# Kernel tuning notes

Measured on AMD Instinct MI355X. Metric: run time of the kernel, lower is better.

Reference implementation:

```python
import jax, jax.numpy as jnp
import numpy as np

N, D, H, F = 50000, 128, 8, 512
HD = D // H
EPS_BN = 1e-5


def _batchnorm(x, gamma, beta):
    # BatchNorm1d in training mode: per-feature batch stats over node dim
    m = x.mean(axis=0)
    v = x.var(axis=0)
    return (x - m) * jax.lax.rsqrt(v + EPS_BN) * gamma + beta


def setup_inputs() -> dict:
    key = jax.random.key(0)
    ks = jax.random.split(key, 12)
    s = 0.05
    return {
        "src": jax.random.normal(ks[0], (N, D), jnp.float32),
        "edge_index": jax.random.randint(ks[1], (2, 800000), 0, N, jnp.int64),
        "q_w": jax.random.normal(ks[2], (D, D), jnp.float32) * s,
        "q_b": jnp.zeros((D,), jnp.float32),
        "k_w": jax.random.normal(ks[3], (D, D), jnp.float32) * s,
        "v_w": jax.random.normal(ks[4], (D, D), jnp.float32) * s,
        "out_w": jax.random.normal(ks[5], (D, D), jnp.float32) * s,
        "out_b": jnp.zeros((D,), jnp.float32),
        "g1": jnp.ones((D,), jnp.float32),
        "b1": jnp.zeros((D,), jnp.float32),
        "lin1_w": jax.random.normal(ks[6], (F, D), jnp.float32) * s,
        "lin1_b": jnp.zeros((F,), jnp.float32),
        "lin2_w": jax.random.normal(ks[7], (D, F), jnp.float32) * s,
        "lin2_b": jnp.zeros((D,), jnp.float32),
        "g2": jnp.ones((D,), jnp.float32),
        "b2": jnp.zeros((D,), jnp.float32),
    }


def reference(src, edge_index, q_w, q_b, k_w, v_w, out_w, out_b,
              g1, b1, lin1_w, lin1_b, lin2_w, lin2_b, g2, b2):
    n = src.shape[0]
    # add self loops, then attention edge index is (dst=edge[1], src=edge[0])
    loops = jnp.arange(n, dtype=edge_index.dtype)
    ei = jnp.concatenate([edge_index, jnp.stack([loops, loops])], axis=1)
    e_src, e_dst = ei[0], ei[1]  # message flows e_src -> e_dst; query index = e_dst

    scaling = float(HD) ** (-0.5)
    q = ((src @ q_w.T + q_b) * scaling).reshape(n, H, HD)
    k = (src @ k_w.T).reshape(n, H, HD)
    v = (src @ v_w.T).reshape(n, H, HD)

    # per-edge scores [E, H]
    w = jnp.einsum("ehd,ehd->eh", q[e_dst], k[e_src])
    # deterministic segment softmax over edges grouped by destination node
    mx = jax.ops.segment_max(w, e_dst, num_segments=n)
    ex = jnp.exp(w - mx[e_dst])
    den = jax.ops.segment_sum(ex, e_dst, num_segments=n)
    attn_w = ex / (den[e_dst] + 1e-16)  # [E, H]

    # weighted scatter-add aggregation -> [n, H, HD]
    msgs = attn_w[:, :, None] * v[e_src]
    agg = jax.ops.segment_sum(msgs, e_dst, num_segments=n)

    attn_out = agg.reshape(n, D) @ out_w.T + out_b
    x = _batchnorm(src + attn_out, g1, b1)

    ff = jax.nn.leaky_relu(x @ lin1_w.T + lin1_b, negative_slope=0.01)
    ff = ff @ lin2_w.T + lin2_b
    x = _batchnorm(x + ff, g2, b2)
    return x
```

## Files before the change

### kernel.cpp

```cpp
#include <hip/hip_runtime.h>
#include <math.h>

#define D 128
#define H 8
#define HD 16

typedef __attribute__((ext_vector_type(8))) short bf16x8;
typedef __attribute__((ext_vector_type(4))) float f32x4;

__device__ __forceinline__ ushort f2bf(float x) {
    union { float f; unsigned u; } v; v.f = x;
    unsigned r = v.u + 0x7fffu + ((v.u >> 16) & 1u);
    return (ushort)(r >> 16);
}
__device__ __forceinline__ float bflo(unsigned u) {
    union { unsigned u; float f; } x; x.u = u << 16; return x.f;
}
__device__ __forceinline__ float bfhi(unsigned u) {
    union { unsigned u; float f; } x; x.u = u & 0xffff0000u; return x.f;
}
__device__ __forceinline__ float bf2f(short s) {
    union { unsigned u; float f; } x; x.u = ((unsigned)(ushort)s) << 16; return x.f;
}

__device__ __forceinline__ float dot16(const float* qf, uint4 a, uint4 b) {
    float w;
    w  = qf[0]  * bflo(a.x) + qf[1]  * bfhi(a.x);
    w += qf[2]  * bflo(a.y) + qf[3]  * bfhi(a.y);
    w += qf[4]  * bflo(a.z) + qf[5]  * bfhi(a.z);
    w += qf[6]  * bflo(a.w) + qf[7]  * bfhi(a.w);
    w += qf[8]  * bflo(b.x) + qf[9]  * bfhi(b.x);
    w += qf[10] * bflo(b.y) + qf[11] * bfhi(b.y);
    w += qf[12] * bflo(b.z) + qf[13] * bfhi(b.z);
    w += qf[14] * bflo(b.w) + qf[15] * bfhi(b.w);
    return w;
}
__device__ __forceinline__ void acc16(float* num, float e, uint4 a, uint4 b) {
    num[0]  = fmaf(e, bflo(a.x), num[0]);  num[1]  = fmaf(e, bfhi(a.x), num[1]);
    num[2]  = fmaf(e, bflo(a.y), num[2]);  num[3]  = fmaf(e, bfhi(a.y), num[3]);
    num[4]  = fmaf(e, bflo(a.z), num[4]);  num[5]  = fmaf(e, bfhi(a.z), num[5]);
    num[6]  = fmaf(e, bflo(a.w), num[6]);  num[7]  = fmaf(e, bfhi(a.w), num[7]);
    num[8]  = fmaf(e, bflo(b.x), num[8]);  num[9]  = fmaf(e, bfhi(b.x), num[9]);
    num[10] = fmaf(e, bflo(b.y), num[10]); num[11] = fmaf(e, bfhi(b.y), num[11]);
    num[12] = fmaf(e, bflo(b.z), num[12]); num[13] = fmaf(e, bfhi(b.z), num[13]);
    num[14] = fmaf(e, bflo(b.w), num[14]); num[15] = fmaf(e, bfhi(b.w), num[15]);
}

template<int AMODE, int EPI, int K, int M>
__global__ __launch_bounds__(256)
void gemm_v3_kernel(const void* __restrict__ Ap,
                    const ushort* __restrict__ W,
                    const float* __restrict__ bias,
                    const void* __restrict__ extra,
                    const float* __restrict__ rawstats,
                    const float* __restrict__ gg,
                    const float* __restrict__ bb,
                    ushort* __restrict__ outb,
                    int N)
{
    constexpr int KC  = (K < 128) ? K : 128;
    constexpr int KT  = KC / 32;
    constexpr int NKC = K / KC;

    __shared__ ushort Bs[128 * 128];
    __shared__ float scs[128], shs[128];

    const int tid = threadIdx.x;
    const int lane = tid & 63, wave = tid >> 6;
    const int lr = lane & 15, lq = lane >> 4;
    const int row0 = blockIdx.x * 32;
    const int colbase = blockIdx.y * 128;

    int ar0 = min(row0 + lr, N - 1);
    int ar1 = min(row0 + 16 + lr, N - 1);

    if (AMODE == 2 && tid < 128) {
        float mean = rawstats[tid] / (float)N;
        float var  = rawstats[128 + tid] / (float)N - mean * mean;
        float sc = gg[tid] * rsqrtf(var + 1e-5f);
        scs[tid] = sc;
        shs[tid] = bb[tid] - mean * sc;
    }

    bf16x8 afr[2][KT];
    bf16x8 araw[2][KT];

    auto loadAraw = [&](int kc) {
        #pragma unroll
        for (int s = 0; s < 2; ++s) {
            int ar = s ? ar1 : ar0;
            if (AMODE == 1) {
                const float* ap = (const float*)Ap + (size_t)ar * K + lq * 8;
                #pragma unroll
                for (int t = 0; t < KT; ++t) {
                    float4 f0 = *(const float4*)(ap + t * 32);
                    float4 f1 = *(const float4*)(ap + t * 32 + 4);
                    bf16x8 o;
                    o[0] = (short)f2bf(f0.x); o[1] = (short)f2bf(f0.y);
                    o[2] = (short)f2bf(f0.z); o[3] = (short)f2bf(f0.w);
                    o[4] = (short)f2bf(f1.x); o[5] = (short)f2bf(f1.y);
                    o[6] = (short)f2bf(f1.z); o[7] = (short)f2bf(f1.w);
                    afr[s][t] = o;
                }
            } else {
                const ushort* ap = (const ushort*)Ap + (size_t)ar * K + kc * KC + lq * 8;
                #pragma unroll
                for (int t = 0; t < KT; ++t) {
                    bf16x8 raw = *(const bf16x8*)(ap + t * 32);
                    if (AMODE == 0) afr[s][t] = raw;
                    else            araw[s][t] = raw;
                }
            }
        }
    };

    auto stageB = [&](int kc) {
        #pragma unroll
        for (int it = 0; it < 8; ++it) {
            int idx = tid + it * 256;
            int c = idx >> 4, u = idx & 15;
            const uint4* gp = (const uint4*)(W + (size_t)(colbase + c) * K + kc * KC) + u;
            *(uint4*)&Bs[c * 128 + 8 * (u ^ (c & 7))] = *gp;
        }
    };

    const float*  extf = (const float*)extra;
    const ushort* extb = (const ushort*)extra;

    f32x4 acc[2][2] = {};

    #pragma unroll 1
    for (int kc = 0; kc < NKC; ++kc) {
        loadAraw(kc);
        if (kc > 0) __syncthreads();
        stageB(kc);
        __syncthreads();

        if (AMODE == 2) {
            #pragma unroll
            for (int s = 0; s < 2; ++s)
                #pragma unroll
                for (int t = 0; t < KT; ++t) {
                    bf16x8 raw = araw[s][t];
                    int kb = t * 32 + lq * 8;
                    bf16x8 o;
                    #pragma unroll
                    for (int e = 0; e < 8; ++e)
                        o[e] = (short)f2bf(fmaf(bf2f(raw[e]), scs[kb + e], shs[kb + e]));
                    afr[s][t] = o;
                }
        }

        const int cl0 = wave * 32 + lr;
        const int cl1 = cl0 + 16;
        #pragma unroll
        for (int t = 0; t < KT; ++t) {
            int u = t * 4 + lq;
            bf16x8 b0 = *(const bf16x8*)&Bs[cl0 * 128 + 8 * (u ^ (cl0 & 7))];
            bf16x8 b1 = *(const bf16x8*)&Bs[cl1 * 128 + 8 * (u ^ (cl1 & 7))];
            acc[0][0] = __builtin_amdgcn_mfma_f32_16x16x32_bf16(afr[0][t], b0, acc[0][0], 0, 0, 0);
            acc[1][0] = __builtin_amdgcn_mfma_f32_16x16x32_bf16(afr[1][t], b0, acc[1][0], 0, 0, 0);
            acc[0][1] = __builtin_amdgcn_mfma_f32_16x16x32_bf16(afr[0][t], b1, acc[0][1], 0, 0, 0);
            acc[1][1] = __builtin_amdgcn_mfma_f32_16x16x32_bf16(afr[1][t], b1, acc[1][1], 0, 0, 0);
        }
    }

    #pragma unroll
    for (int ct = 0; ct < 2; ++ct) {
        int gcol = colbase + wave * 32 + ct * 16 + lr;
        float biasv = bias[gcol];
        float scv = 0.f, shv = 0.f;
        if (EPI == 4) {
            float mean = rawstats[gcol] / (float)N;
            float var  = rawstats[128 + gcol] / (float)N - mean * mean;
            scv = gg[gcol] * rsqrtf(var + 1e-5f);
            shv = bb[gcol] - mean * scv;
        }
        #pragma unroll
        for (int s = 0; s < 2; ++s) {
            #pragma unroll
            for (int r = 0; r < 4; ++r) {
                int grow = row0 + s * 16 + lq * 4 + r;
                if (grow >= N) continue;
                size_t o = (size_t)grow * M + gcol;
                float v = acc[s][ct][r] + biasv;
                if (EPI == 2)      v = v > 0.f ? v : 0.01f * v;
                else if (EPI == 3) v += extf[o];
                else if (EPI == 4) v += fmaf(bf2f((short)extb[o]), scv, shv);
                outb[o] = f2bf(v);
            }
        }
    }
}

__global__ __launch_bounds__(256)
void convert_deg_kernel(const float* __restrict__ qw, const float* __restrict__ qb,
                        const float* __restrict__ kw, const float* __restrict__ vw,
                        const float* __restrict__ ow, const float* __restrict__ w1,
                        const float* __restrict__ w2,
                        ushort* __restrict__ wqkv, ushort* __restrict__ wout,
                        ushort* __restrict__ w1b, ushort* __restrict__ w2b,
                        float* __restrict__ bqkv,
                        const int* __restrict__ ei, long long E0,
                        int* __restrict__ deg)
{
    long long i = (long long)blockIdx.x * 256 + threadIdx.x;
    if (i < E0) atomicAdd(&deg[ei[E0 + i]], 1);
    if (i < 49152) {
        int row = (int)i >> 7;
        float v;
        if (row < 128)      v = 0.25f * qw[i];
        else if (row < 256) v = kw[i - 16384];
        else                v = vw[i - 32768];
        wqkv[i] = f2bf(v);
        return;
    }
    long long j = i - 49152;
    if (j < 16384) { wout[j] = f2bf(ow[j]); return; }
    j -= 16384;
    if (j < 65536) { w1b[j] = f2bf(w1[j]); return; }
    j -= 65536;
    if (j < 65536) { w2b[j] = f2bf(w2[j]); return; }
    j -= 65536;
    if (j < 384) bqkv[j] = (j < 128) ? 0.25f * qb[j] : 0.f;
}

__global__ __launch_bounds__(256)
void scan_block_sum(const int* __restrict__ deg, int n, int* __restrict__ bsum)
{
    __shared__ int sh[256];
    int i = blockIdx.x * 256 + threadIdx.x;
    sh[threadIdx.x] = (i < n) ? deg[i] : 0;
    __syncthreads();
    for (int ofs = 128; ofs > 0; ofs >>= 1) {
        if (threadIdx.x < ofs) sh[threadIdx.x] += sh[threadIdx.x + ofs];
        __syncthreads();
    }
    if (threadIdx.x == 0) bsum[blockIdx.x] = sh[0];
}

__global__ __launch_bounds__(256)
void scan_final(const int* __restrict__ deg, int n, const int* __restrict__ bsum,
                int nb, int* __restrict__ rowptr)
{
    __shared__ int sb[256];
    __shared__ int sh[256];
    int t = threadIdx.x;
    sb[t] = (t < nb) ? bsum[t] : 0;
    __syncthreads();
    for (int ofs = 1; ofs < 256; ofs <<= 1) {
        int v = (t >= ofs) ? sb[t - ofs] : 0;
        __syncthreads();
        sb[t] += v;
        __syncthreads();
    }
    int boff = (blockIdx.x == 0) ? 0 : sb[blockIdx.x - 1];

    int i = blockIdx.x * 256 + t;
    int v = (i < n) ? deg[i] : 0;
    sh[t] = v;
    __syncthreads();
    for (int ofs = 1; ofs < 256; ofs <<= 1) {
        int u = (t >= ofs) ? sh[t - ofs] : 0;
        __syncthreads();
        sh[t] += u;
        __syncthreads();
    }
    if (i < n) rowptr[i] = boff + sh[t] - v;
    if (i == n - 1) rowptr[n] = boff + sh[t];
}

__global__ __launch_bounds__(256)
void scatter_kernel(const int* __restrict__ ei, long long E0,
                    const int* __restrict__ rowptr, int* __restrict__ cnt,
                    int* __restrict__ col)
{
    long long e = (long long)blockIdx.x * 256 + threadIdx.x;
    if (e >= E0) return;
    int s = ei[e], d = ei[E0 + e];
    int pos = rowptr[d] + atomicAdd(&cnt[d], 1);
    col[pos] = s;
}

__global__ __launch_bounds__(256)
void gat_agg_kernel(const int* __restrict__ rowptr, const int* __restrict__ col,
                    const ushort* __restrict__ qkv, ushort* __restrict__ agg, int N)
{
    int node = blockIdx.x * 4 + (threadIdx.x >> 6);
    if (node >= N) return;
    int lane = threadIdx.x & 63;
    int es = lane >> 3, h = lane & 7;
    const uint4* Q = (const uint4*)qkv;

    const uint4* qp = Q + (size_t)node * 48 + h * 2;
    uint4 qa = qp[0], qb = qp[1];
    float qf[16];
    qf[0]=bflo(qa.x); qf[1]=bfhi(qa.x); qf[2]=bflo(qa.y); qf[3]=bfhi(qa.y);
    qf[4]=bflo(qa.z); qf[5]=bfhi(qa.z); qf[6]=bflo(qa.w); qf[7]=bfhi(qa.w);
    qf[8]=bflo(qb.x); qf[9]=bfhi(qb.x); qf[10]=bflo(qb.y); qf[11]=bfhi(qb.y);
    qf[12]=bflo(qb.z); qf[13]=bfhi(qb.z); qf[14]=bflo(qb.w); qf[15]=bfhi(qb.w);

    float num[16];
    #pragma unroll
    for (int i = 0; i < 16; i++) num[i] = 0.f;
    float den = 0.f;

    int beg = rowptr[node];
    int total = rowptr[node + 1] - beg + 1;
    for (int idx = es; idx < total; idx += 8) {
        int s = (idx == 0) ? node : col[beg + idx - 1];
        const uint4* rp = Q + (size_t)s * 48 + h * 2;
        uint4 ka = rp[16], kb = rp[17], va = rp[32], vb = rp[33];
        float ev = __expf(dot16(qf, ka, kb));
        den += ev;
        acc16(num, ev, va, vb);
    }

    #pragma unroll
    for (int m = 8; m < 64; m <<= 1) {
        den += __shfl_xor(den, m, 64);
        #pragma unroll
        for (int i = 0; i < 16; i++) num[i] += __shfl_xor(num[i], m, 64);
    }

    if (es == 0) {
        float inv = 1.f / (den + 1e-16f);
        uint4 o0, o1;
        o0.x = (uint)f2bf(num[0]*inv)  | ((uint)f2bf(num[1]*inv)  << 16);
        o0.y = (uint)f2bf(num[2]*inv)  | ((uint)f2bf(num[3]*inv)  << 16);
        o0.z = (uint)f2bf(num[4]*inv)  | ((uint)f2bf(num[5]*inv)  << 16);
        o0.w = (uint)f2bf(num[6]*inv)  | ((uint)f2bf(num[7]*inv)  << 16);
        o1.x = (uint)f2bf(num[8]*inv)  | ((uint)f2bf(num[9]*inv)  << 16);
        o1.y = (uint)f2bf(num[10]*inv) | ((uint)f2bf(num[11]*inv) << 16);
        o1.z = (uint)f2bf(num[12]*inv) | ((uint)f2bf(num[13]*inv) << 16);
        o1.w = (uint)f2bf(num[14]*inv) | ((uint)f2bf(num[15]*inv) << 16);
        uint4* op = (uint4*)(agg + (size_t)node * 128 + h * 16);
        op[0] = o0; op[1] = o1;
    }
}

__global__ __launch_bounds__(256)
void bn_stats_bf16_kernel(const ushort* __restrict__ y, int N, float* __restrict__ stats)
{
    int jp = threadIdx.x & 63;
    int q4 = threadIdx.x >> 6;
    int r = blockIdx.x * 256 + q4;
    int rend = min(N, (int)(blockIdx.x + 1) * 256);
    float s0 = 0.f, qq0 = 0.f, s1 = 0.f, qq1 = 0.f;
    const uint* yp = (const uint*)y;
    for (; r < rend; r += 4) {
        uint u = yp[(size_t)r * 64 + jp];
        float a = bflo(u), b = bfhi(u);
        s0 += a; qq0 += a * a; s1 += b; qq1 += b * b;
    }
    __shared__ float sh[4][64][4];
    sh[q4][jp][0] = s0; sh[q4][jp][1] = qq0; sh[q4][jp][2] = s1; sh[q4][jp][3] = qq1;
    __syncthreads();
    if (threadIdx.x < 128) {
        int p = threadIdx.x >> 1;
        int w = threadIdx.x & 1;
        float ss = 0.f, sq = 0.f;
        #pragma unroll
        for (int i = 0; i < 4; i++) { ss += sh[i][p][w * 2]; sq += sh[i][p][w * 2 + 1]; }
        unsafeAtomicAdd(&stats[2 * p + w], ss);
        unsafeAtomicAdd(&stats[128 + 2 * p + w], sq);
    }
}

__global__ __launch_bounds__(256)
void bn_apply_out_kernel(const ushort* __restrict__ y, const float* __restrict__ rawstats,
                         const float* __restrict__ g, const float* __restrict__ b,
                         float* __restrict__ out, int total4, int N)
{
    __shared__ float scs[128], shs[128];
    if (threadIdx.x < 128) {
        int j = threadIdx.x;
        float mean = rawstats[j] / (float)N;
        float var  = rawstats[128 + j] / (float)N - mean * mean;
        float sc = g[j] * rsqrtf(var + 1e-5f);
        scs[j] = sc;
        shs[j] = b[j] - mean * sc;
    }
    __syncthreads();
    int i = blockIdx.x * 256 + threadIdx.x;
    if (i >= total4) return;
    uint2 u = reinterpret_cast<const uint2*>(y)[i];
    int j = (i * 4) & (D - 1);
    float4 v;
    v.x = bflo(u.x) * scs[j + 0] + shs[j + 0];
    v.y = bfhi(u.x) * scs[j + 1] + shs[j + 1];
    v.z = bflo(u.y) * scs[j + 2] + shs[j + 2];
    v.w = bfhi(u.y) * scs[j + 3] + shs[j + 3];
    reinterpret_cast<float4*>(out)[i] = v;
}

extern "C" void kernel_launch(void* const* d_in, const int* in_sizes, int n_in,
                              void* d_out, int out_size, void* d_ws, size_t ws_size,
                              hipStream_t stream)
{
    const float* src    = (const float*)d_in[0];
    const int*   ei     = (const int*)  d_in[1];
    const float* q_w    = (const float*)d_in[2];
    const float* q_b    = (const float*)d_in[3];
    const float* k_w    = (const float*)d_in[4];
    const float* v_w    = (const float*)d_in[5];
    const float* out_w  = (const float*)d_in[6];
    const float* out_b  = (const float*)d_in[7];
    const float* g1     = (const float*)d_in[8];
    const float* b1     = (const float*)d_in[9];
    const float* lin1_w = (const float*)d_in[10];
    const float* lin1_b = (const float*)d_in[11];
    const float* lin2_w = (const float*)d_in[12];
    const float* lin2_b = (const float*)d_in[13];
    const float* g2     = (const float*)d_in[14];
    const float* b2     = (const float*)d_in[15];

    const int N        = in_sizes[0] / D;
    const long long E0 = in_sizes[1] / 2;

    float* ws = (float*)d_ws;
    size_t off = 0;
    ushort* qkv  = (ushort*)(ws + off); off += (size_t)N * 192;
    ushort* agg  = (ushort*)(ws + off); off += (size_t)N * 64;
    ushort* y1b  = (ushort*)(ws + off); off += (size_t)N * 64;
    ushort* hid  = (ushort*)(ws + off); off += (size_t)N * 256;
    ushort* y2b  = (ushort*)(ws + off); off += (size_t)N * 64;
    ushort* wqkv = (ushort*)(ws + off); off += 24576;
    ushort* woutb= (ushort*)(ws + off); off += 8192;
    ushort* w1b  = (ushort*)(ws + off); off += 32768;
    ushort* w2b  = (ushort*)(ws + off); off += 32768;
    float*  bqkv = ws + off;            off += 384;
    size_t zero_start = off;
    int* deg    = (int*)(ws + off); off += N;
    int* cnt    = (int*)(ws + off); off += N;
    float* stats1 = ws + off; off += 512;
    float* stats2 = ws + off; off += 512;
    size_t zero_cnt = off - zero_start;
    int* rowptr = (int*)(ws + off); off += N + 1;
    int* bsum   = (int*)(ws + off); off += 256;
    int* col    = (int*)(ws + off); off += E0;

    hipMemsetAsync(ws + zero_start, 0, zero_cnt * sizeof(float), stream);

    dim3 blk(256);

    dim3 gE0((unsigned)((E0 + 255) / 256));
    hipLaunchKernelGGL(convert_deg_kernel, gE0, blk, 0, stream,
                       q_w, q_b, k_w, v_w, out_w, lin1_w, lin2_w,
                       wqkv, woutb, w1b, w2b, bqkv, ei, E0, deg);

    int nb = (N + 255) / 256;
    hipLaunchKernelGGL(scan_block_sum, dim3(nb), blk, 0, stream, deg, N, bsum);
    hipLaunchKernelGGL(scan_final, dim3(nb), blk, 0, stream, deg, N, bsum, nb, rowptr);
    hipLaunchKernelGGL(scatter_kernel, gE0, blk, 0, stream, ei, E0, rowptr, cnt, col);

    int gx = (N + 31) / 32;

    hipLaunchKernelGGL((gemm_v3_kernel<1, 0, 128, 384>), dim3(gx, 3), blk, 0, stream,
                       src, wqkv, bqkv, nullptr, nullptr, nullptr, nullptr, qkv, N);

    hipLaunchKernelGGL(gat_agg_kernel, dim3((N + 3) / 4), blk, 0, stream,
                       rowptr, col, qkv, agg, N);

    hipLaunchKernelGGL((gemm_v3_kernel<0, 3, 128, 128>), dim3(gx, 1), blk, 0, stream,
                       agg, woutb, out_b, src, nullptr, nullptr, nullptr, y1b, N);

    dim3 gS((N + 255) / 256);
    hipLaunchKernelGGL(bn_stats_bf16_kernel, gS, blk, 0, stream, y1b, N, stats1);

    hipLaunchKernelGGL((gemm_v3_kernel<2, 2, 128, 512>), dim3(gx, 4), blk, 0, stream,
                       y1b, w1b, lin1_b, nullptr, stats1, g1, b1, hid, N);

    hipLaunchKernelGGL((gemm_v3_kernel<0, 4, 512, 128>), dim3(gx, 1), blk, 0, stream,
                       hid, w2b, lin2_b, y1b, stats1, g1, b1, y2b, N);

    hipLaunchKernelGGL(bn_stats_bf16_kernel, gS, blk, 0, stream, y2b, N, stats2);
    int total4 = N * D / 4;
    hipLaunchKernelGGL(bn_apply_out_kernel, dim3((total4 + 255) / 256), blk, 0, stream,
                       y2b, stats2, g2, b2, (float*)d_out, total4, N);
}
```

Measured before the change: 475.9 us.

## Hold GEMM weights in registers with persistent row loop and fold BN1 into lin1

Result: faster. 447.5 us (-6.0%).

```diff
diff --git a/kernel.cpp b/kernel.cpp
--- a/kernel.cpp
+++ b/kernel.cpp
@@ -46,118 +46,134 @@
     num[14] = fmaf(e, bflo(b.w), num[14]); num[15] = fmaf(e, bfhi(b.w), num[15]);
 }
 
-template<int AMODE, int EPI, int K, int M>
-__global__ __launch_bounds__(256)
-void gemm_v3_kernel(const void* __restrict__ Ap,
+template<int EPI, int M>
+__global__ __launch_bounds__(256)
+void gemm_v4_kernel(const ushort* __restrict__ A,
                     const ushort* __restrict__ W,
                     const float* __restrict__ bias,
-                    const void* __restrict__ extra,
+                    const float* __restrict__ extf,
+                    ushort* __restrict__ outb, int N)
+{
+    const int lane = threadIdx.x & 63, wave = threadIdx.x >> 6;
+    const int lr = lane & 15, lq = lane >> 4;
+    const int colbase = blockIdx.y * 128 + wave * 32;
+
+    bf16x8 bfr[2][4];
+    {
+        const ushort* wp = W + (size_t)(colbase + lr) * 128 + lq * 8;
+        #pragma unroll
+        for (int ct = 0; ct < 2; ++ct)
+            #pragma unroll
+            for (int t = 0; t < 4; ++t)
+                bfr[ct][t] = *(const bf16x8*)(wp + (size_t)ct * 16 * 128 + t * 32);
+    }
+    float biasv[2];
+    biasv[0] = bias[colbase + lr];
+    biasv[1] = bias[colbase + 16 + lr];
+
+    const int stride = gridDim.x * 32;
+    int r0 = blockIdx.x * 32;
+    if (r0 >= N) return;
+
+    bf16x8 cur[2][4], nxt[2][4];
+    auto loadA = [&](int rb, bf16x8 (&dst)[2][4]) {
+        #pragma unroll
+        for (int s = 0; s < 2; ++s) {
+            int ar = min(rb + s * 16 + lr, N - 1);
+            const ushort* ap = A + (size_t)ar * 128 + lq * 8;
+            #pragma unroll
+            for (int t = 0; t < 4; ++t)
+                dst[s][t] = *(const bf16x8*)(ap + t * 32);
+        }
+    };
+    loadA(r0, cur);
+
+    while (true) {
+        int rn = r0 + stride;
+        if (rn < N) loadA(rn, nxt);
+
+        f32x4 acc[2][2] = {};
+        #pragma unroll
+        for (int t = 0; t < 4; ++t) {
+            acc[0][0] = __builtin_amdgcn_mfma_f32_16x16x32_bf16(cur[0][t], bfr[0][t], acc[0][0], 0, 0, 0);
+            acc[1][0] = __builtin_amdgcn_mfma_f32_16x16x32_bf16(cur[1][t], bfr[0][t], acc[1][0], 0, 0, 0);
+            acc[0][1] = __builtin_amdgcn_mfma_f32_16x16x32_bf16(cur[0][t], bfr[1][t], acc[0][1], 0, 0, 0);
+            acc[1][1] = __builtin_amdgcn_mfma_f32_16x16x32_bf16(cur[1][t], bfr[1][t], acc[1][1], 0, 0, 0);
+        }
+
+        #pragma unroll
+        for (int ct = 0; ct < 2; ++ct) {
+            int gcol = colbase + ct * 16 + lr;
+            #pragma unroll
+            for (int s = 0; s < 2; ++s) {
+                #pragma unroll
+                for (int r = 0; r < 4; ++r) {
+                    int grow = r0 + s * 16 + lq * 4 + r;
+                    if (grow >= N) continue;
+                    size_t o = (size_t)grow * M + gcol;
+                    float v = acc[s][ct][r] + biasv[ct];
+                    if (EPI == 2)      v = v > 0.f ? v : 0.01f * v;
+                    else if (EPI == 3) v += extf[o];
+                    outb[o] = f2bf(v);
+                }
+            }
+        }
+
+        if (rn >= N) break;
+        r0 = rn;
+        #pragma unroll
+        for (int s = 0; s < 2; ++s)
+            #pragma unroll
+            for (int t = 0; t < 4; ++t) cur[s][t] = nxt[s][t];
+    }
+}
+
+template<int K, int MW>
+__global__ __launch_bounds__(256)
+void gemm_v2_kernel(const ushort* __restrict__ Ap,
+                    const ushort* __restrict__ W,
+                    const float* __restrict__ bias,
+                    const ushort* __restrict__ extb,
                     const float* __restrict__ rawstats,
                     const float* __restrict__ gg,
                     const float* __restrict__ bb,
                     ushort* __restrict__ outb,
                     int N)
 {
-    constexpr int KC  = (K < 128) ? K : 128;
+    constexpr int M   = MW * 4;
+    constexpr int KC  = 128;
     constexpr int KT  = KC / 32;
     constexpr int NKC = K / KC;
 
-    __shared__ ushort Bs[128 * 128];
-    __shared__ float scs[128], shs[128];
-
-    const int tid = threadIdx.x;
-    const int lane = tid & 63, wave = tid >> 6;
+    const int lane = threadIdx.x & 63, wave = threadIdx.x >> 6;
     const int lr = lane & 15, lq = lane >> 4;
     const int row0 = blockIdx.x * 32;
-    const int colbase = blockIdx.y * 128;
+    const int c0w  = wave * MW;
 
     int ar0 = min(row0 + lr, N - 1);
     int ar1 = min(row0 + 16 + lr, N - 1);
 
-    if (AMODE == 2 && tid < 128) {
-        float mean = rawstats[tid] / (float)N;
-        float var  = rawstats[128 + tid] / (float)N - mean * mean;
-        float sc = gg[tid] * rsqrtf(var + 1e-5f);
-        scs[tid] = sc;
-        shs[tid] = bb[tid] - mean * sc;
-    }
-
     bf16x8 afr[2][KT];
-    bf16x8 araw[2][KT];
-
-    auto loadAraw = [&](int kc) {
+    auto loadA = [&](int kc) {
         #pragma unroll
         for (int s = 0; s < 2; ++s) {
             int ar = s ? ar1 : ar0;
-            if (AMODE == 1) {
-                const float* ap = (const float*)Ap + (size_t)ar * K + lq * 8;
-                #pragma unroll
-                for (int t = 0; t < KT; ++t) {
-                    float4 f0 = *(const float4*)(ap + t * 32);
-                    float4 f1 = *(const float4*)(ap + t * 32 + 4);
-                    bf16x8 o;
-                    o[0] = (short)f2bf(f0.x); o[1] = (short)f2bf(f0.y);
-                    o[2] = (short)f2bf(f0.z); o[3] = (short)f2bf(f0.w);
-                    o[4] = (short)f2bf(f1.x); o[5] = (short)f2bf(f1.y);
-                    o[6] = (short)f2bf(f1.z); o[7] = (short)f2bf(f1.w);
-                    afr[s][t] = o;
-                }
-            } else {
-                const ushort* ap = (const ushort*)Ap + (size_t)ar * K + kc * KC + lq * 8;
-                #pragma unroll
-                for (int t = 0; t < KT; ++t) {
-                    bf16x8 raw = *(const bf16x8*)(ap + t * 32);
-                    if (AMODE == 0) afr[s][t] = raw;
-                    else            araw[s][t] = raw;
-                }
-            }
+            const ushort* ap = Ap + (size_t)ar * K + kc * KC + lq * 8;
+            #pragma unroll
+            for (int t = 0; t < KT; ++t) afr[s][t] = *(const bf16x8*)(ap + t * 32);
         }
     };
 
-    auto stageB = [&](int kc) {
-        #pragma unroll
-        for (int it = 0; it < 8; ++it) {
-            int idx = tid + it * 256;
-            int c = idx >> 4, u = idx & 15;
-            const uint4* gp = (const uint4*)(W + (size_t)(colbase + c) * K + kc * KC) + u;
-            *(uint4*)&Bs[c * 128 + 8 * (u ^ (c & 7))] = *gp;
-        }
-    };
-
-    const float*  extf = (const float*)extra;
-    const ushort* extb = (const ushort*)extra;
-
     f32x4 acc[2][2] = {};
-
     #pragma unroll 1
     for (int kc = 0; kc < NKC; ++kc) {
-        loadAraw(kc);
-        if (kc > 0) __syncthreads();
-        stageB(kc);
-        __syncthreads();
-
-        if (AMODE == 2) {
-            #pragma unroll
-            for (int s = 0; s < 2; ++s)
-                #pragma unroll
-                for (int t = 0; t < KT; ++t) {
-                    bf16x8 raw = araw[s][t];
-                    int kb = t * 32 + lq * 8;
-                    bf16x8 o;
-                    #pragma unroll
-                    for (int e = 0; e < 8; ++e)
-                        o[e] = (short)f2bf(fmaf(bf2f(raw[e]), scs[kb + e], shs[kb + e]));
-                    afr[s][t] = o;
-                }
-        }
-
-        const int cl0 = wave * 32 + lr;
-        const int cl1 = cl0 + 16;
+        loadA(kc);
+        const ushort* wp0 = W + (size_t)(c0w + lr) * K + kc * KC + lq * 8;
+        const ushort* wp1 = wp0 + (size_t)16 * K;
         #pragma unroll
         for (int t = 0; t < KT; ++t) {
-            int u = t * 4 + lq;
-            bf16x8 b0 = *(const bf16x8*)&Bs[cl0 * 128 + 8 * (u ^ (cl0 & 7))];
-            bf16x8 b1 = *(const bf16x8*)&Bs[cl1 * 128 + 8 * (u ^ (cl1 & 7))];
+            bf16x8 b0 = *(const bf16x8*)(wp0 + t * 32);
+            bf16x8 b1 = *(const bf16x8*)(wp1 + t * 32);
             acc[0][0] = __builtin_amdgcn_mfma_f32_16x16x32_bf16(afr[0][t], b0, acc[0][0], 0, 0, 0);
             acc[1][0] = __builtin_amdgcn_mfma_f32_16x16x32_bf16(afr[1][t], b0, acc[1][0], 0, 0, 0);
             acc[0][1] = __builtin_amdgcn_mfma_f32_16x16x32_bf16(afr[0][t], b1, acc[0][1], 0, 0, 0);
@@ -167,26 +183,20 @@
 
     #pragma unroll
     for (int ct = 0; ct < 2; ++ct) {
-        int gcol = colbase + wave * 32 + ct * 16 + lr;
-        float biasv = bias[gcol];
-        float scv = 0.f, shv = 0.f;
-        if (EPI == 4) {
-            float mean = rawstats[gcol] / (float)N;
-            float var  = rawstats[128 + gcol] / (float)N - mean * mean;
-            scv = gg[gcol] * rsqrtf(var + 1e-5f);
-            shv = bb[gcol] - mean * scv;
-        }
+        int col = c0w + ct * 16 + lr;
+        float biasv = bias[col];
+        float mean = rawstats[col] / (float)N;
+        float var  = rawstats[128 + col] / (float)N - mean * mean;
+        float scv = gg[col] * rsqrtf(var + 1e-5f);
+        float shv = bb[col] - mean * scv;
         #pragma unroll
         for (int s = 0; s < 2; ++s) {
             #pragma unroll
             for (int r = 0; r < 4; ++r) {
                 int grow = row0 + s * 16 + lq * 4 + r;
                 if (grow >= N) continue;
-                size_t o = (size_t)grow * M + gcol;
-                float v = acc[s][ct][r] + biasv;
-                if (EPI == 2)      v = v > 0.f ? v : 0.01f * v;
-                else if (EPI == 3) v += extf[o];
-                else if (EPI == 4) v += fmaf(bf2f((short)extb[o]), scv, shv);
+                size_t o = (size_t)grow * M + col;
+                float v = acc[s][ct][r] + biasv + fmaf(bf2f((short)extb[o]), scv, shv);
                 outb[o] = f2bf(v);
             }
         }
@@ -201,11 +211,21 @@
                         ushort* __restrict__ wqkv, ushort* __restrict__ wout,
                         ushort* __restrict__ w1b, ushort* __restrict__ w2b,
                         float* __restrict__ bqkv,
+                        const float* __restrict__ src, ushort* __restrict__ srcbf,
+                        int nd8,
                         const int* __restrict__ ei, long long E0,
                         int* __restrict__ deg)
 {
     long long i = (long long)blockIdx.x * 256 + threadIdx.x;
     if (i < E0) atomicAdd(&deg[ei[E0 + i]], 1);
+    if (i < nd8) {
+        const float4* sp = (const float4*)(src + i * 8);
+        float4 f0 = sp[0], f1 = sp[1];
+        ushort u[8];
+        u[0]=f2bf(f0.x); u[1]=f2bf(f0.y); u[2]=f2bf(f0.z); u[3]=f2bf(f0.w);
+        u[4]=f2bf(f1.x); u[5]=f2bf(f1.y); u[6]=f2bf(f1.z); u[7]=f2bf(f1.w);
+        *(uint4*)(srcbf + i * 8) = *(uint4*)u;
+    }
     if (i < 49152) {
         int row = (int)i >> 7;
         float v;
@@ -223,6 +243,35 @@
     if (j < 65536) { w2b[j] = f2bf(w2[j]); return; }
     j -= 65536;
     if (j < 384) bqkv[j] = (j < 128) ? 0.25f * qb[j] : 0.f;
+}
+
+__global__ __launch_bounds__(256)
+void w1fold_kernel(const ushort* __restrict__ w1b, const float* __restrict__ lb1,
+                   const float* __restrict__ rawstats,
+                   const float* __restrict__ g1, const float* __restrict__ b1,
+                   ushort* __restrict__ w1f, float* __restrict__ bias1f, int N)
+{
+    int f = blockIdx.x * 4 + (threadIdx.x >> 6);
+    int lane = threadIdx.x & 63;
+    int k0 = lane * 2;
+    float m0 = rawstats[k0] / (float)N;
+    float v0 = rawstats[128 + k0] / (float)N - m0 * m0;
+    float sc0 = g1[k0] * rsqrtf(v0 + 1e-5f);
+    float sh0 = b1[k0] - m0 * sc0;
+    float m1 = rawstats[k0 + 1] / (float)N;
+    float v1 = rawstats[128 + k0 + 1] / (float)N - m1 * m1;
+    float sc1 = g1[k0 + 1] * rsqrtf(v1 + 1e-5f);
+    float sh1 = b1[k0 + 1] - m1 * sc1;
+
+    uint wp = *(const uint*)(w1b + (size_t)f * 128 + k0);
+    float w0 = bflo(wp), w1v = bfhi(wp);
+    uint o = (uint)f2bf(w0 * sc0) | ((uint)f2bf(w1v * sc1) << 16);
+    *(uint*)(w1f + (size_t)f * 128 + k0) = o;
+
+    float part = w0 * sh0 + w1v * sh1;
+    #pragma unroll
+    for (int m = 1; m < 64; m <<= 1) part += __shfl_xor(part, m, 64);
+    if (lane == 0) bias1f[f] = lb1[f] + part;
 }
 
 __global__ __launch_bounds__(256)
@@ -420,16 +469,19 @@
 
     float* ws = (float*)d_ws;
     size_t off = 0;
-    ushort* qkv  = (ushort*)(ws + off); off += (size_t)N * 192;
-    ushort* agg  = (ushort*)(ws + off); off += (size_t)N * 64;
-    ushort* y1b  = (ushort*)(ws + off); off += (size_t)N * 64;
-    ushort* hid  = (ushort*)(ws + off); off += (size_t)N * 256;
-    ushort* y2b  = (ushort*)(ws + off); off += (size_t)N * 64;
-    ushort* wqkv = (ushort*)(ws + off); off += 24576;
-    ushort* woutb= (ushort*)(ws + off); off += 8192;
-    ushort* w1b  = (ushort*)(ws + off); off += 32768;
-    ushort* w2b  = (ushort*)(ws + off); off += 32768;
-    float*  bqkv = ws + off;            off += 384;
+    ushort* qkv   = (ushort*)(ws + off); off += (size_t)N * 192;
+    ushort* agg   = (ushort*)(ws + off); off += (size_t)N * 64;
+    ushort* srcbf = (ushort*)(ws + off); off += (size_t)N * 64;
+    ushort* y1b   = (ushort*)(ws + off); off += (size_t)N * 64;
+    ushort* hid   = (ushort*)(ws + off); off += (size_t)N * 256;
+    ushort* y2b   = (ushort*)(ws + off); off += (size_t)N * 64;
+    ushort* wqkv  = (ushort*)(ws + off); off += 24576;
+    ushort* woutb = (ushort*)(ws + off); off += 8192;
+    ushort* w1b   = (ushort*)(ws + off); off += 32768;
+    ushort* w1f   = (ushort*)(ws + off); off += 32768;
+    ushort* w2b   = (ushort*)(ws + off); off += 32768;
+    float*  bqkv  = ws + off;            off += 384;
+    float*  bias1f= ws + off;            off += 512;
     size_t zero_start = off;
     int* deg    = (int*)(ws + off); off += N;
     int* cnt    = (int*)(ws + off); off += N;
@@ -447,31 +499,35 @@
     dim3 gE0((unsigned)((E0 + 255) / 256));
     hipLaunchKernelGGL(convert_deg_kernel, gE0, blk, 0, stream,
                        q_w, q_b, k_w, v_w, out_w, lin1_w, lin2_w,
-                       wqkv, woutb, w1b, w2b, bqkv, ei, E0, deg);
+                       wqkv, woutb, w1b, w2b, bqkv,
+                       src, srcbf, N * 16, ei, E0, deg);
 
     int nb = (N + 255) / 256;
     hipLaunchKernelGGL(scan_block_sum, dim3(nb), blk, 0, stream, deg, N, bsum);
     hipLaunchKernelGGL(scan_final, dim3(nb), blk, 0, stream, deg, N, bsum, nb, rowptr);
     hipLaunchKernelGGL(scatter_kernel, gE0, blk, 0, stream, ei, E0, rowptr, cnt, col);
 
-    int gx = (N + 31) / 32;
-
-    hipLaunchKernelGGL((gemm_v3_kernel<1, 0, 128, 384>), dim3(gx, 3), blk, 0, stream,
-                       src, wqkv, bqkv, nullptr, nullptr, nullptr, nullptr, qkv, N);
+    const int gx = 1024;
+
+    hipLaunchKernelGGL((gemm_v4_kernel<0, 384>), dim3(gx, 3), blk, 0, stream,
+                       srcbf, wqkv, bqkv, nullptr, qkv, N);
 
     hipLaunchKernelGGL(gat_agg_kernel, dim3((N + 3) / 4), blk, 0, stream,
                        rowptr, col, qkv, agg, N);
 
-    hipLaunchKernelGGL((gemm_v3_kernel<0, 3, 128, 128>), dim3(gx, 1), blk, 0, stream,
-                       agg, woutb, out_b, src, nullptr, nullptr, nullptr, y1b, N);
+    hipLaunchKernelGGL((gemm_v4_kernel<3, 128>), dim3(gx, 1), blk, 0, stream,
+                       agg, woutb, out_b, src, y1b, N);
 
     dim3 gS((N + 255) / 256);
     hipLaunchKernelGGL(bn_stats_bf16_kernel, gS, blk, 0, stream, y1b, N, stats1);
 
-    hipLaunchKernelGGL((gemm_v3_kernel<2, 2, 128, 512>), dim3(gx, 4), blk, 0, stream,
-                       y1b, w1b, lin1_b, nullptr, stats1, g1, b1, hid, N);
-
-    hipLaunchKernelGGL((gemm_v3_kernel<0, 4, 512, 128>), dim3(gx, 1), blk, 0, stream,
+    hipLaunchKernelGGL(w1fold_kernel, dim3(128), blk, 0, stream,
+                       w1b, lin1_b, stats1, g1, b1, w1f, bias1f, N);
+
+    hipLaunchKernelGGL((gemm_v4_kernel<2, 512>), dim3(gx, 4), blk, 0, stream,
+                       y1b, w1f, bias1f, nullptr, hid, N);
+
+    hipLaunchKernelGGL((gemm_v2_kernel<512, 32>), dim3((N + 31) / 32), blk, 0, stream,
                        hid, w2b, lin2_b, y1b, stats1, g1, b1, y2b, N);
 
     hipLaunchKernelGGL(bn_stats_bf16_kernel, gS, blk, 0, stream, y2b, N, stats2);
```
